# Performance work log

Measured on AMD Instinct MI355X. Metric: run time of the kernel, lower is better.

## Reference

```python
import jax, jax.numpy as jnp
import numpy as np

B, N, NB, C, CZ = 4, 1024, 32, 384, 128
EPS = 1e-6


def setup_inputs() -> dict:
    key = jax.random.key(0)
    k1, k2, k3, k4, k5 = jax.random.split(key, 5)
    s_i = jax.random.normal(k1, (B, N, C), dtype=jnp.float32)
    s_ij = jax.random.normal(k2, (B, N, NB, C), dtype=jnp.float32)
    m_ij = jnp.ones((B, N, NB), dtype=jnp.float32)
    z_ij = jax.random.normal(k3, (B, N, NB, CZ), dtype=jnp.float32)
    W_s = jax.random.normal(k4, (C, C), dtype=jnp.float32) / np.sqrt(C)
    W_z = jax.random.normal(k5, (CZ, C), dtype=jnp.float32) / np.sqrt(CZ)
    gamma = jnp.ones((C,), dtype=jnp.float32)
    beta = jnp.zeros((C,), dtype=jnp.float32)
    return {"s_i": s_i, "s_ij": s_ij, "m_ij": m_ij, "z_ij": z_ij,
            "W_s": W_s, "W_z": W_z, "gamma": gamma, "beta": beta}


def reference(s_i, s_ij, m_ij, z_ij, W_s, W_z, gamma, beta):
    # Dense projection of neighbor single act: (B,N,n,C) @ (C,C)
    s_proj = jnp.einsum('bnkc,cd->bnkd', s_ij, W_s)
    # subtract center single act
    diff = s_proj - s_i[..., None, :]
    # gate by projected pair act: (B,N,n,Cz) @ (Cz,C)
    gate = jnp.einsum('bnkz,zd->bnkd', z_ij, W_z)
    msg = diff * gate
    # masked sum over neighbor axis
    s_new = jnp.sum(msg * m_ij[..., None], axis=-2)  # (B,N,C)
    # layernorm over last axis
    mu = jnp.mean(s_new, axis=-1, keepdims=True)
    var = jnp.mean(jnp.square(s_new - mu), axis=-1, keepdims=True)
    s_new = (s_new - mu) * jax.lax.rsqrt(var + EPS) * gamma + beta
    return s_new
```

## Files before the change

kernel.cpp:

```cpp
#include <hip/hip_runtime.h>
#include <hip/hip_bf16.h>

#define B_ 4
#define N_ 1024
#define NB_ 32
#define C_ 384
#define CZ_ 128
#define NSITES (B_ * N_)
#define EPSV 1e-6f
#define PAD 40
#define SPB 2
#define MR 64
#define THREADS 512

typedef unsigned short u16;
typedef unsigned int u32;
typedef __bf16 bf16x8 __attribute__((ext_vector_type(8)));
typedef float f32x4 __attribute__((ext_vector_type(4)));

__device__ __forceinline__ u16 f2bf(float f) {
    return __builtin_bit_cast(u16, __float2bfloat16(f));
}
__device__ __forceinline__ u32 pk2(float lo, float hi) {
    return ((u32)f2bf(hi) << 16) | f2bf(lo);
}
__device__ __forceinline__ float bfbits2f(u16 u) {
    union { float f; u32 i; } x;
    x.i = ((u32)u) << 16;
    return x.f;
}

__global__ void prep_weights(const float* __restrict__ Ws, const float* __restrict__ Wz,
                             u16* __restrict__ Wts, u16* __restrict__ Wtz) {
    int idx = blockIdx.x * 256 + threadIdx.x;
    if (idx < C_ * C_) {
        int d = idx / C_, c = idx % C_;
        Wts[idx] = f2bf(Ws[c * C_ + d]);
    } else {
        int j = idx - C_ * C_;
        if (j < C_ * CZ_) {
            int d = j / CZ_, z = j % CZ_;
            Wtz[j] = f2bf(Wz[z * C_ + d]);
        }
    }
}

__global__ __launch_bounds__(THREADS, 4)
void fused_msg_kernel(const float* __restrict__ s_i,
                      const float* __restrict__ s_ij,
                      const float* __restrict__ m_ij,
                      const float* __restrict__ z_ij,
                      const u16* __restrict__ Wts,
                      const u16* __restrict__ Wtz,
                      const float* __restrict__ gamma,
                      const float* __restrict__ beta,
                      float* __restrict__ out) {
    __shared__ u16 ldsW[2][C_ * PAD];
    __shared__ u16 ldsA[2][MR * PAD];
    __shared__ float lds_snew[SPB * C_];

    const int tid = threadIdx.x;
    const int wave = tid >> 6;
    const int lane = tid & 63;
    const int q = lane >> 4;
    const int ln = lane & 15;
    const int mg = wave >> 2;
    const int cb = (wave & 3) * 96;

    const int site0 = blockIdx.x * SPB;
    const long rowbase = (long)site0 * NB_;

    const int arow = tid >> 3, aseg = tid & 7;
    const int wrow = tid >> 2, wseg = tid & 3;
    const int la_w = arow * PAD + aseg * 4;
    const int lw_w = wrow * PAD + wseg * 8;

    const float mv = m_ij[rowbase + lane];

    const f32x4 ZERO = {0.f, 0.f, 0.f, 0.f};
    f32x4 acc[2][6];
    #pragma unroll
    for (int mt = 0; mt < 2; ++mt)
        #pragma unroll
        for (int nt = 0; nt < 6; ++nt)
            acc[mt][nt] = ZERO;

    float4 ra;
    uint4 rw0, rw1, rw2;

    {
        const int kd = CZ_;
        const float* ap = z_ij + (rowbase + arow) * kd + aseg * 4;
        const u16* wp = Wtz + wrow * kd + wseg * 8;
        const int ws1 = 128 * kd, ws2 = 256 * kd;

        ra = *reinterpret_cast<const float4*>(ap);
        rw0 = *reinterpret_cast<const uint4*>(wp);
        rw1 = *reinterpret_cast<const uint4*>(wp + ws1);
        rw2 = *reinterpret_cast<const uint4*>(wp + ws2);
        ap += 32; wp += 32;
        {
            uint2 a2 = {pk2(ra.x, ra.y), pk2(ra.z, ra.w)};
            *reinterpret_cast<uint2*>(&ldsA[0][la_w]) = a2;
            *reinterpret_cast<uint4*>(&ldsW[0][lw_w]) = rw0;
            *reinterpret_cast<uint4*>(&ldsW[0][lw_w + 128 * PAD]) = rw1;
            *reinterpret_cast<uint4*>(&ldsW[0][lw_w + 256 * PAD]) = rw2;
        }
        __syncthreads();

        #pragma unroll 2
        for (int c = 0; c < 4; ++c) {
            if (c + 1 < 4) {
                ra = *reinterpret_cast<const float4*>(ap);
                rw0 = *reinterpret_cast<const uint4*>(wp);
                rw1 = *reinterpret_cast<const uint4*>(wp + ws1);
                rw2 = *reinterpret_cast<const uint4*>(wp + ws2);
                ap += 32; wp += 32;
            }
            const u16* lA = ldsA[c & 1];
            const u16* lW = ldsW[c & 1];
            bf16x8 a0 = *reinterpret_cast<const bf16x8*>(&lA[(mg * 32 + ln) * PAD + q * 8]);
            bf16x8 a1 = *reinterpret_cast<const bf16x8*>(&lA[(mg * 32 + 16 + ln) * PAD + q * 8]);
            #pragma unroll
            for (int nt = 0; nt < 6; ++nt) {
                bf16x8 b = *reinterpret_cast<const bf16x8*>(&lW[(cb + nt * 16 + ln) * PAD + q * 8]);
                acc[0][nt] = __builtin_amdgcn_mfma_f32_16x16x32_bf16(a0, b, acc[0][nt], 0, 0, 0);
                acc[1][nt] = __builtin_amdgcn_mfma_f32_16x16x32_bf16(a1, b, acc[1][nt], 0, 0, 0);
            }
            if (c + 1 < 4) {
                int nb = (c + 1) & 1;
                uint2 a2 = {pk2(ra.x, ra.y), pk2(ra.z, ra.w)};
                *reinterpret_cast<uint2*>(&ldsA[nb][la_w]) = a2;
                *reinterpret_cast<uint4*>(&ldsW[nb][lw_w]) = rw0;
                *reinterpret_cast<uint4*>(&ldsW[nb][lw_w + 128 * PAD]) = rw1;
                *reinterpret_cast<uint4*>(&ldsW[nb][lw_w + 256 * PAD]) = rw2;
            }
            __syncthreads();
        }
    }

    u32 gateb[2][6][2];
    #pragma unroll
    for (int mt = 0; mt < 2; ++mt) {
        int rb = mg * 32 + mt * 16 + q * 4;
        float m0 = __shfl(mv, rb + 0, 64);
        float m1 = __shfl(mv, rb + 1, 64);
        float m2 = __shfl(mv, rb + 2, 64);
        float m3 = __shfl(mv, rb + 3, 64);
        #pragma unroll
        for (int nt = 0; nt < 6; ++nt) {
            gateb[mt][nt][0] = pk2(acc[mt][nt][0] * m0, acc[mt][nt][1] * m1);
            gateb[mt][nt][1] = pk2(acc[mt][nt][2] * m2, acc[mt][nt][3] * m3);
            acc[mt][nt] = ZERO;
        }
    }

    {
        const int kd = C_;
        const float* ap = s_ij + (rowbase + arow) * kd + aseg * 4;
        const u16* wp = Wts + wrow * kd + wseg * 8;
        const int ws1 = 128 * kd, ws2 = 256 * kd;

        ra = *reinterpret_cast<const float4*>(ap);
        rw0 = *reinterpret_cast<const uint4*>(wp);
        rw1 = *reinterpret_cast<const uint4*>(wp + ws1);
        rw2 = *reinterpret_cast<const uint4*>(wp + ws2);
        ap += 32; wp += 32;
        {
            uint2 a2 = {pk2(ra.x, ra.y), pk2(ra.z, ra.w)};
            *reinterpret_cast<uint2*>(&ldsA[0][la_w]) = a2;
            *reinterpret_cast<uint4*>(&ldsW[0][lw_w]) = rw0;
            *reinterpret_cast<uint4*>(&ldsW[0][lw_w + 128 * PAD]) = rw1;
            *reinterpret_cast<uint4*>(&ldsW[0][lw_w + 256 * PAD]) = rw2;
        }
        __syncthreads();

        #pragma unroll 2
        for (int c = 0; c < 12; ++c) {
            if (c + 1 < 12) {
                ra = *reinterpret_cast<const float4*>(ap);
                rw0 = *reinterpret_cast<const uint4*>(wp);
                rw1 = *reinterpret_cast<const uint4*>(wp + ws1);
                rw2 = *reinterpret_cast<const uint4*>(wp + ws2);
                ap += 32; wp += 32;
            }
            const u16* lA = ldsA[c & 1];
            const u16* lW = ldsW[c & 1];
            bf16x8 a0 = *reinterpret_cast<const bf16x8*>(&lA[(mg * 32 + ln) * PAD + q * 8]);
            bf16x8 a1 = *reinterpret_cast<const bf16x8*>(&lA[(mg * 32 + 16 + ln) * PAD + q * 8]);
            #pragma unroll
            for (int nt = 0; nt < 6; ++nt) {
                bf16x8 b = *reinterpret_cast<const bf16x8*>(&lW[(cb + nt * 16 + ln) * PAD + q * 8]);
                acc[0][nt] = __builtin_amdgcn_mfma_f32_16x16x32_bf16(a0, b, acc[0][nt], 0, 0, 0);
                acc[1][nt] = __builtin_amdgcn_mfma_f32_16x16x32_bf16(a1, b, acc[1][nt], 0, 0, 0);
            }
            if (c + 1 < 12) {
                int nb = (c + 1) & 1;
                uint2 a2 = {pk2(ra.x, ra.y), pk2(ra.z, ra.w)};
                *reinterpret_cast<uint2*>(&ldsA[nb][la_w]) = a2;
                *reinterpret_cast<uint4*>(&ldsW[nb][lw_w]) = rw0;
                *reinterpret_cast<uint4*>(&ldsW[nb][lw_w + 128 * PAD]) = rw1;
                *reinterpret_cast<uint4*>(&ldsW[nb][lw_w + 256 * PAD]) = rw2;
            }
            __syncthreads();
        }
    }

    #pragma unroll
    for (int nt = 0; nt < 6; ++nt) {
        int col = cb + nt * 16 + ln;
        float si = s_i[(long)(site0 + mg) * C_ + col];
        float p = 0.f;
        #pragma unroll
        for (int mt = 0; mt < 2; ++mt) {
            #pragma unroll
            for (int r = 0; r < 4; ++r) {
                float g = bfbits2f((u16)(gateb[mt][nt][r >> 1] >> ((r & 1) * 16)));
                p += (acc[mt][nt][r] - si) * g;
            }
        }
        p += __shfl_xor(p, 16, 64);
        p += __shfl_xor(p, 32, 64);
        if (q == 0) lds_snew[mg * C_ + col] = p;
    }
    __syncthreads();

    if (wave < SPB) {
        const int site = wave;
        float v[6];
        float sum = 0.f, sumsq = 0.f;
        #pragma unroll
        for (int i = 0; i < 6; ++i) {
            v[i] = lds_snew[site * C_ + lane + i * 64];
            sum += v[i];
            sumsq += v[i] * v[i];
        }
        #pragma unroll
        for (int off = 32; off >= 1; off >>= 1) {
            sum += __shfl_xor(sum, off, 64);
            sumsq += __shfl_xor(sumsq, off, 64);
        }
        float mu = sum * (1.f / C_);
        float var = sumsq * (1.f / C_) - mu * mu;
        float rs = rsqrtf(var + EPSV);
        #pragma unroll
        for (int i = 0; i < 6; ++i) {
            int col = lane + i * 64;
            out[(long)(site0 + site) * C_ + col] = (v[i] - mu) * rs * gamma[col] + beta[col];
        }
    }
}

extern "C" void kernel_launch(void* const* d_in, const int* in_sizes, int n_in,
                              void* d_out, int out_size, void* d_ws, size_t ws_size,
                              hipStream_t stream) {
    (void)in_sizes; (void)n_in; (void)out_size; (void)ws_size;
    const float* s_i   = (const float*)d_in[0];
    const float* s_ij  = (const float*)d_in[1];
    const float* m_ij  = (const float*)d_in[2];
    const float* z_ij  = (const float*)d_in[3];
    const float* W_s   = (const float*)d_in[4];
    const float* W_z   = (const float*)d_in[5];
    const float* gamma = (const float*)d_in[6];
    const float* beta  = (const float*)d_in[7];
    float* out = (float*)d_out;

    u16* wts = (u16*)d_ws;
    u16* wtz = wts + C_ * C_;

    int prep_elems = C_ * C_ + C_ * CZ_;
    prep_weights<<<(prep_elems + 255) / 256, 256, 0, stream>>>(W_s, W_z, wts, wtz);
    fused_msg_kernel<<<NSITES / SPB, THREADS, 0, stream>>>(s_i, s_ij, m_ij, z_ij, wts, wtz,
                                                           gamma, beta, out);
}
```

Measured before the change: 438.7 us.

## Stage weights via global_load_lds and load activations straight into MFMA registers

Weights are pre-laid-out in chunked, fragment-order bf16 so each K-chunk can be copied into LDS with direct global-to-LDS loads, with no register round trip. Activation fragments are read from global straight into registers in MFMA operand layout and converted there, removing the LDS staging of the A operand and its bank traffic. LDS use per block drops, which may help occupancy. In exchange each lane now issues scattered per-row float4 loads of the activations, which may coalesce worse than the earlier contiguous row loads.

Measured after the change: 468.1 us. 6.7% more time.

```diff
diff --git a/kernel.cpp b/kernel.cpp
--- a/kernel.cpp
+++ b/kernel.cpp
@@ -8,10 +8,11 @@
 #define CZ_ 128
 #define NSITES (B_ * N_)
 #define EPSV 1e-6f
-#define PAD 40
 #define SPB 2
-#define MR 64
 #define THREADS 512
+#define WCHUNK_B 24576
+#define NKS 12
+#define NKZ 4
 
 typedef unsigned short u16;
 typedef unsigned int u32;
@@ -29,18 +30,31 @@
     x.i = ((u32)u) << 16;
     return x.f;
 }
+__device__ __forceinline__ bf16x8 mk8(float4 lo, float4 hi) {
+    union { u32 u[4]; bf16x8 v; } x;
+    x.u[0] = pk2(lo.x, lo.y); x.u[1] = pk2(lo.z, lo.w);
+    x.u[2] = pk2(hi.x, hi.y); x.u[3] = pk2(hi.z, hi.w);
+    return x.v;
+}
 
 __global__ void prep_weights(const float* __restrict__ Ws, const float* __restrict__ Wz,
-                             u16* __restrict__ Wts, u16* __restrict__ Wtz) {
+                             u16* __restrict__ wsS, u16* __restrict__ wsZ) {
     int idx = blockIdx.x * 256 + threadIdx.x;
-    if (idx < C_ * C_) {
-        int d = idx / C_, c = idx % C_;
-        Wts[idx] = f2bf(Ws[c * C_ + d]);
+    const int NS = NKS * 4 * C_ * 8;
+    if (idx < NS) {
+        int e = idx & 7, t = idx >> 3;
+        int d = t % C_, u = t / C_;
+        int q = u & 3, c = u >> 2;
+        int k = c * 32 + q * 8 + e;
+        wsS[idx] = f2bf(Ws[k * C_ + d]);
     } else {
-        int j = idx - C_ * C_;
-        if (j < C_ * CZ_) {
-            int d = j / CZ_, z = j % CZ_;
-            Wtz[j] = f2bf(Wz[z * C_ + d]);
+        int j = idx - NS;
+        if (j < NKZ * 4 * C_ * 8) {
+            int e = j & 7, t = j >> 3;
+            int d = t % C_, u = t / C_;
+            int q = u & 3, c = u >> 2;
+            int k = c * 32 + q * 8 + e;
+            wsZ[j] = f2bf(Wz[k * C_ + d]);
         }
     }
 }
@@ -50,13 +64,12 @@
                       const float* __restrict__ s_ij,
                       const float* __restrict__ m_ij,
                       const float* __restrict__ z_ij,
-                      const u16* __restrict__ Wts,
-                      const u16* __restrict__ Wtz,
+                      const u16* __restrict__ wsS,
+                      const u16* __restrict__ wsZ,
                       const float* __restrict__ gamma,
                       const float* __restrict__ beta,
                       float* __restrict__ out) {
-    __shared__ u16 ldsW[2][C_ * PAD];
-    __shared__ u16 ldsA[2][MR * PAD];
+    __shared__ u16 ldsW[2][WCHUNK_B / 2];
     __shared__ float lds_snew[SPB * C_];
 
     const int tid = threadIdx.x;
@@ -69,11 +82,7 @@
 
     const int site0 = blockIdx.x * SPB;
     const long rowbase = (long)site0 * NB_;
-
-    const int arow = tid >> 3, aseg = tid & 7;
-    const int wrow = tid >> 2, wseg = tid & 3;
-    const int la_w = arow * PAD + aseg * 4;
-    const int lw_w = wrow * PAD + wseg * 8;
+    const long arow0 = rowbase + mg * 32 + ln;
 
     const float mv = m_ij[rowbase + lane];
 
@@ -85,59 +94,61 @@
         for (int nt = 0; nt < 6; ++nt)
             acc[mt][nt] = ZERO;
 
-    float4 ra;
-    uint4 rw0, rw1, rw2;
-
-    {
-        const int kd = CZ_;
-        const float* ap = z_ij + (rowbase + arow) * kd + aseg * 4;
-        const u16* wp = Wtz + wrow * kd + wseg * 8;
-        const int ws1 = 128 * kd, ws2 = 256 * kd;
-
-        ra = *reinterpret_cast<const float4*>(ap);
-        rw0 = *reinterpret_cast<const uint4*>(wp);
-        rw1 = *reinterpret_cast<const uint4*>(wp + ws1);
-        rw2 = *reinterpret_cast<const uint4*>(wp + ws2);
-        ap += 32; wp += 32;
-        {
-            uint2 a2 = {pk2(ra.x, ra.y), pk2(ra.z, ra.w)};
-            *reinterpret_cast<uint2*>(&ldsA[0][la_w]) = a2;
-            *reinterpret_cast<uint4*>(&ldsW[0][lw_w]) = rw0;
-            *reinterpret_cast<uint4*>(&ldsW[0][lw_w + 128 * PAD]) = rw1;
-            *reinterpret_cast<uint4*>(&ldsW[0][lw_w + 256 * PAD]) = rw2;
-        }
+    float4 ra[2][4];
+    const int ldsq = q * (C_ * 8);
+
+#define STAGE_W(wsbase, c, buf) do {                                          \
+        const char* _s = (const char*)(wsbase) + (c) * WCHUNK_B;              \
+        char* _d = (char*)&ldsW[(buf)][0];                                    \
+        _Pragma("unroll")                                                     \
+        for (int _i = 0; _i < 3; ++_i) {                                      \
+            int _o = _i * 8192 + tid * 16;                                    \
+            __builtin_amdgcn_global_load_lds(                                 \
+                (const __attribute__((address_space(1))) void*)(_s + _o),     \
+                (__attribute__((address_space(3))) void*)(_d + _o),           \
+                16, 0, 0);                                                    \
+        }                                                                     \
+    } while (0)
+
+#define LOAD_A(base, kd, c, sl) do {                                          \
+        const float* _p0 = (base) + arow0 * (kd) + (c) * 32 + q * 8;          \
+        const float* _p1 = _p0 + 16 * (kd);                                   \
+        ra[sl][0] = *reinterpret_cast<const float4*>(_p0);                    \
+        ra[sl][1] = *reinterpret_cast<const float4*>(_p0 + 4);                \
+        ra[sl][2] = *reinterpret_cast<const float4*>(_p1);                    \
+        ra[sl][3] = *reinterpret_cast<const float4*>(_p1 + 4);                \
+    } while (0)
+
+#define COMPUTE(sl) do {                                                      \
+        bf16x8 _a0 = mk8(ra[sl][0], ra[sl][1]);                               \
+        bf16x8 _a1 = mk8(ra[sl][2], ra[sl][3]);                               \
+        const u16* _lw = &ldsW[sl][ldsq];                                     \
+        _Pragma("unroll")                                                     \
+        for (int _nt = 0; _nt < 6; ++_nt) {                                   \
+            bf16x8 _b = *reinterpret_cast<const bf16x8*>(                     \
+                _lw + (cb + _nt * 16 + ln) * 8);                              \
+            acc[0][_nt] = __builtin_amdgcn_mfma_f32_16x16x32_bf16(            \
+                _a0, _b, acc[0][_nt], 0, 0, 0);                               \
+            acc[1][_nt] = __builtin_amdgcn_mfma_f32_16x16x32_bf16(            \
+                _a1, _b, acc[1][_nt], 0, 0, 0);                               \
+        }                                                                     \
+    } while (0)
+
+    STAGE_W(wsZ, 0, 0);
+    LOAD_A(z_ij, CZ_, 0, 0);
+    __syncthreads();
+    #pragma unroll
+    for (int c = 0; c < NKZ; ++c) {
+        if (c + 1 < NKZ) {
+            STAGE_W(wsZ, c + 1, (c + 1) & 1);
+            LOAD_A(z_ij, CZ_, c + 1, (c + 1) & 1);
+        }
+        COMPUTE(c & 1);
         __syncthreads();
-
-        #pragma unroll 2
-        for (int c = 0; c < 4; ++c) {
-            if (c + 1 < 4) {
-                ra = *reinterpret_cast<const float4*>(ap);
-                rw0 = *reinterpret_cast<const uint4*>(wp);
-                rw1 = *reinterpret_cast<const uint4*>(wp + ws1);
-                rw2 = *reinterpret_cast<const uint4*>(wp + ws2);
-                ap += 32; wp += 32;
-            }
-            const u16* lA = ldsA[c & 1];
-            const u16* lW = ldsW[c & 1];
-            bf16x8 a0 = *reinterpret_cast<const bf16x8*>(&lA[(mg * 32 + ln) * PAD + q * 8]);
-            bf16x8 a1 = *reinterpret_cast<const bf16x8*>(&lA[(mg * 32 + 16 + ln) * PAD + q * 8]);
-            #pragma unroll
-            for (int nt = 0; nt < 6; ++nt) {
-                bf16x8 b = *reinterpret_cast<const bf16x8*>(&lW[(cb + nt * 16 + ln) * PAD + q * 8]);
-                acc[0][nt] = __builtin_amdgcn_mfma_f32_16x16x32_bf16(a0, b, acc[0][nt], 0, 0, 0);
-                acc[1][nt] = __builtin_amdgcn_mfma_f32_16x16x32_bf16(a1, b, acc[1][nt], 0, 0, 0);
-            }
-            if (c + 1 < 4) {
-                int nb = (c + 1) & 1;
-                uint2 a2 = {pk2(ra.x, ra.y), pk2(ra.z, ra.w)};
-                *reinterpret_cast<uint2*>(&ldsA[nb][la_w]) = a2;
-                *reinterpret_cast<uint4*>(&ldsW[nb][lw_w]) = rw0;
-                *reinterpret_cast<uint4*>(&ldsW[nb][lw_w + 128 * PAD]) = rw1;
-                *reinterpret_cast<uint4*>(&ldsW[nb][lw_w + 256 * PAD]) = rw2;
-            }
-            __syncthreads();
-        }
-    }
+    }
+
+    STAGE_W(wsS, 0, 0);
+    LOAD_A(s_ij, C_, 0, 0);
 
     u32 gateb[2][6][2];
     #pragma unroll
@@ -154,57 +165,21 @@
             acc[mt][nt] = ZERO;
         }
     }
-
-    {
-        const int kd = C_;
-        const float* ap = s_ij + (rowbase + arow) * kd + aseg * 4;
-        const u16* wp = Wts + wrow * kd + wseg * 8;
-        const int ws1 = 128 * kd, ws2 = 256 * kd;
-
-        ra = *reinterpret_cast<const float4*>(ap);
-        rw0 = *reinterpret_cast<const uint4*>(wp);
-        rw1 = *reinterpret_cast<const uint4*>(wp + ws1);
-        rw2 = *reinterpret_cast<const uint4*>(wp + ws2);
-        ap += 32; wp += 32;
-        {
-            uint2 a2 = {pk2(ra.x, ra.y), pk2(ra.z, ra.w)};
-            *reinterpret_cast<uint2*>(&ldsA[0][la_w]) = a2;
-            *reinterpret_cast<uint4*>(&ldsW[0][lw_w]) = rw0;
-            *reinterpret_cast<uint4*>(&ldsW[0][lw_w + 128 * PAD]) = rw1;
-            *reinterpret_cast<uint4*>(&ldsW[0][lw_w + 256 * PAD]) = rw2;
-        }
+    __syncthreads();
+
+    #pragma unroll
+    for (int c = 0; c < NKS; ++c) {
+        if (c + 1 < NKS) {
+            STAGE_W(wsS, c + 1, (c + 1) & 1);
+            LOAD_A(s_ij, C_, c + 1, (c + 1) & 1);
+        }
+        COMPUTE(c & 1);
         __syncthreads();
-
-        #pragma unroll 2
-        for (int c = 0; c < 12; ++c) {
-            if (c + 1 < 12) {
-                ra = *reinterpret_cast<const float4*>(ap);
-                rw0 = *reinterpret_cast<const uint4*>(wp);
-                rw1 = *reinterpret_cast<const uint4*>(wp + ws1);
-                rw2 = *reinterpret_cast<const uint4*>(wp + ws2);
-                ap += 32; wp += 32;
-            }
-            const u16* lA = ldsA[c & 1];
-            const u16* lW = ldsW[c & 1];
-            bf16x8 a0 = *reinterpret_cast<const bf16x8*>(&lA[(mg * 32 + ln) * PAD + q * 8]);
-            bf16x8 a1 = *reinterpret_cast<const bf16x8*>(&lA[(mg * 32 + 16 + ln) * PAD + q * 8]);
-            #pragma unroll
-            for (int nt = 0; nt < 6; ++nt) {
-                bf16x8 b = *reinterpret_cast<const bf16x8*>(&lW[(cb + nt * 16 + ln) * PAD + q * 8]);
-                acc[0][nt] = __builtin_amdgcn_mfma_f32_16x16x32_bf16(a0, b, acc[0][nt], 0, 0, 0);
-                acc[1][nt] = __builtin_amdgcn_mfma_f32_16x16x32_bf16(a1, b, acc[1][nt], 0, 0, 0);
-            }
-            if (c + 1 < 12) {
-                int nb = (c + 1) & 1;
-                uint2 a2 = {pk2(ra.x, ra.y), pk2(ra.z, ra.w)};
-                *reinterpret_cast<uint2*>(&ldsA[nb][la_w]) = a2;
-                *reinterpret_cast<uint4*>(&ldsW[nb][lw_w]) = rw0;
-                *reinterpret_cast<uint4*>(&ldsW[nb][lw_w + 128 * PAD]) = rw1;
-                *reinterpret_cast<uint4*>(&ldsW[nb][lw_w + 256 * PAD]) = rw2;
-            }
-            __syncthreads();
-        }
-    }
+    }
+
+#undef STAGE_W
+#undef LOAD_A
+#undef COMPUTE
 
     #pragma unroll
     for (int nt = 0; nt < 6; ++nt) {
@@ -265,11 +240,11 @@
     const float* beta  = (const float*)d_in[7];
     float* out = (float*)d_out;
 
-    u16* wts = (u16*)d_ws;
-    u16* wtz = wts + C_ * C_;
-
-    int prep_elems = C_ * C_ + C_ * CZ_;
-    prep_weights<<<(prep_elems + 255) / 256, 256, 0, stream>>>(W_s, W_z, wts, wtz);
-    fused_msg_kernel<<<NSITES / SPB, THREADS, 0, stream>>>(s_i, s_ij, m_ij, z_ij, wts, wtz,
-                                                           gamma, beta, out);
-}
+    u16* wsS = (u16*)d_ws;
+    u16* wsZ = wsS + NKS * 4 * C_ * 8;
+
+    int prep_elems = NKS * 4 * C_ * 8 + NKZ * 4 * C_ * 8;
+    prep_weights<<<(prep_elems + 255) / 256, 256, 0, stream>>>(W_s, W_z, wsS, wsZ);
+    fused_msg_kernel<<<NSITES / SPB, THREADS, 0, stream>>>(s_i, s_ij, m_ij, z_ij,
+                                                           wsS, wsZ, gamma, beta, out);
+}
```

## Pre-swizzle weights into MFMA fragment order and hoist s_ij prefetch over gate packing

Applied to the files above, without the earlier changes.

Weights are reordered at prep time into a chunk/quad/column/8-element layout, so each thread copies contiguous 16-byte runs from global to LDS and the MFMA B operands are read at unpadded contiguous offsets. The A tile in LDS is split into quad-planes with a small pad instead of the row PAD=40 layout. The first s_ij and W_s chunk loads are issued before the gate pack/mask step, so that latency overlaps the conversion work. This cuts LDS footprint and strided global weight reads, but it can change LDS bank-conflict behaviour.

Result: faster. 385.2 us (-12.2%).

```diff
diff --git a/kernel.cpp b/kernel.cpp
--- a/kernel.cpp
+++ b/kernel.cpp
@@ -8,10 +8,13 @@
 #define CZ_ 128
 #define NSITES (B_ * N_)
 #define EPSV 1e-6f
-#define PAD 40
 #define SPB 2
-#define MR 64
 #define THREADS 512
+#define NKZ 4
+#define NKS 12
+#define WCH_U16 12288
+#define APLANE 528
+#define ABUF_U16 (3 * APLANE + 512)
 
 typedef unsigned short u16;
 typedef unsigned int u32;
@@ -31,16 +34,23 @@
 }
 
 __global__ void prep_weights(const float* __restrict__ Ws, const float* __restrict__ Wz,
-                             u16* __restrict__ Wts, u16* __restrict__ Wtz) {
+                             u16* __restrict__ wsS, u16* __restrict__ wsZ) {
     int idx = blockIdx.x * 256 + threadIdx.x;
-    if (idx < C_ * C_) {
-        int d = idx / C_, c = idx % C_;
-        Wts[idx] = f2bf(Ws[c * C_ + d]);
+    const int NS = NKS * 4 * C_ * 8;
+    if (idx < NS) {
+        int e = idx & 7, t = idx >> 3;
+        int d = t % C_, u = t / C_;
+        int q = u & 3, c = u >> 2;
+        int k = c * 32 + q * 8 + e;
+        wsS[idx] = f2bf(Ws[k * C_ + d]);
     } else {
-        int j = idx - C_ * C_;
-        if (j < C_ * CZ_) {
-            int d = j / CZ_, z = j % CZ_;
-            Wtz[j] = f2bf(Wz[z * C_ + d]);
+        int j = idx - NS;
+        if (j < NKZ * 4 * C_ * 8) {
+            int e = j & 7, t = j >> 3;
+            int d = t % C_, u = t / C_;
+            int q = u & 3, c = u >> 2;
+            int k = c * 32 + q * 8 + e;
+            wsZ[j] = f2bf(Wz[k * C_ + d]);
         }
     }
 }
@@ -50,13 +60,13 @@
                       const float* __restrict__ s_ij,
                       const float* __restrict__ m_ij,
                       const float* __restrict__ z_ij,
-                      const u16* __restrict__ Wts,
-                      const u16* __restrict__ Wtz,
+                      const u16* __restrict__ wsS,
+                      const u16* __restrict__ wsZ,
                       const float* __restrict__ gamma,
                       const float* __restrict__ beta,
                       float* __restrict__ out) {
-    __shared__ u16 ldsW[2][C_ * PAD];
-    __shared__ u16 ldsA[2][MR * PAD];
+    __shared__ u16 ldsW[2][WCH_U16];
+    __shared__ u16 ldsA[2][ABUF_U16];
     __shared__ float lds_snew[SPB * C_];
 
     const int tid = threadIdx.x;
@@ -71,9 +81,8 @@
     const long rowbase = (long)site0 * NB_;
 
     const int arow = tid >> 3, aseg = tid & 7;
-    const int wrow = tid >> 2, wseg = tid & 3;
-    const int la_w = arow * PAD + aseg * 4;
-    const int lw_w = wrow * PAD + wseg * 8;
+    const int la_w = (aseg >> 1) * APLANE + arow * 8 + (aseg & 1) * 4;
+    const int lw_w = tid * 8;
 
     const float mv = m_ij[rowbase + lane];
 
@@ -88,56 +97,65 @@
     float4 ra;
     uint4 rw0, rw1, rw2;
 
+    const int ra0 = q * APLANE + (mg * 32 + ln) * 8;
+    const int wq0 = q * 3072;
+
     {
-        const int kd = CZ_;
-        const float* ap = z_ij + (rowbase + arow) * kd + aseg * 4;
-        const u16* wp = Wtz + wrow * kd + wseg * 8;
-        const int ws1 = 128 * kd, ws2 = 256 * kd;
+        const float* ap = z_ij + (rowbase + arow) * CZ_ + aseg * 4;
+        const u16* wp = wsZ + lw_w;
 
         ra = *reinterpret_cast<const float4*>(ap);
         rw0 = *reinterpret_cast<const uint4*>(wp);
-        rw1 = *reinterpret_cast<const uint4*>(wp + ws1);
-        rw2 = *reinterpret_cast<const uint4*>(wp + ws2);
-        ap += 32; wp += 32;
+        rw1 = *reinterpret_cast<const uint4*>(wp + 4096);
+        rw2 = *reinterpret_cast<const uint4*>(wp + 8192);
+        ap += 32; wp += WCH_U16;
         {
             uint2 a2 = {pk2(ra.x, ra.y), pk2(ra.z, ra.w)};
             *reinterpret_cast<uint2*>(&ldsA[0][la_w]) = a2;
             *reinterpret_cast<uint4*>(&ldsW[0][lw_w]) = rw0;
-            *reinterpret_cast<uint4*>(&ldsW[0][lw_w + 128 * PAD]) = rw1;
-            *reinterpret_cast<uint4*>(&ldsW[0][lw_w + 256 * PAD]) = rw2;
+            *reinterpret_cast<uint4*>(&ldsW[0][lw_w + 4096]) = rw1;
+            *reinterpret_cast<uint4*>(&ldsW[0][lw_w + 8192]) = rw2;
         }
         __syncthreads();
 
         #pragma unroll 2
-        for (int c = 0; c < 4; ++c) {
-            if (c + 1 < 4) {
+        for (int c = 0; c < NKZ; ++c) {
+            if (c + 1 < NKZ) {
                 ra = *reinterpret_cast<const float4*>(ap);
                 rw0 = *reinterpret_cast<const uint4*>(wp);
-                rw1 = *reinterpret_cast<const uint4*>(wp + ws1);
-                rw2 = *reinterpret_cast<const uint4*>(wp + ws2);
-                ap += 32; wp += 32;
+                rw1 = *reinterpret_cast<const uint4*>(wp + 4096);
+                rw2 = *reinterpret_cast<const uint4*>(wp + 8192);
+                ap += 32; wp += WCH_U16;
             }
             const u16* lA = ldsA[c & 1];
             const u16* lW = ldsW[c & 1];
-            bf16x8 a0 = *reinterpret_cast<const bf16x8*>(&lA[(mg * 32 + ln) * PAD + q * 8]);
-            bf16x8 a1 = *reinterpret_cast<const bf16x8*>(&lA[(mg * 32 + 16 + ln) * PAD + q * 8]);
+            bf16x8 a0 = *reinterpret_cast<const bf16x8*>(&lA[ra0]);
+            bf16x8 a1 = *reinterpret_cast<const bf16x8*>(&lA[ra0 + 128]);
             #pragma unroll
             for (int nt = 0; nt < 6; ++nt) {
-                bf16x8 b = *reinterpret_cast<const bf16x8*>(&lW[(cb + nt * 16 + ln) * PAD + q * 8]);
+                bf16x8 b = *reinterpret_cast<const bf16x8*>(&lW[wq0 + (cb + nt * 16 + ln) * 8]);
                 acc[0][nt] = __builtin_amdgcn_mfma_f32_16x16x32_bf16(a0, b, acc[0][nt], 0, 0, 0);
                 acc[1][nt] = __builtin_amdgcn_mfma_f32_16x16x32_bf16(a1, b, acc[1][nt], 0, 0, 0);
             }
-            if (c + 1 < 4) {
+            if (c + 1 < NKZ) {
                 int nb = (c + 1) & 1;
                 uint2 a2 = {pk2(ra.x, ra.y), pk2(ra.z, ra.w)};
                 *reinterpret_cast<uint2*>(&ldsA[nb][la_w]) = a2;
                 *reinterpret_cast<uint4*>(&ldsW[nb][lw_w]) = rw0;
-                *reinterpret_cast<uint4*>(&ldsW[nb][lw_w + 128 * PAD]) = rw1;
-                *reinterpret_cast<uint4*>(&ldsW[nb][lw_w + 256 * PAD]) = rw2;
+                *reinterpret_cast<uint4*>(&ldsW[nb][lw_w + 4096]) = rw1;
+                *reinterpret_cast<uint4*>(&ldsW[nb][lw_w + 8192]) = rw2;
             }
             __syncthreads();
         }
     }
+
+    const float* ap = s_ij + (rowbase + arow) * C_ + aseg * 4;
+    const u16* wp = wsS + lw_w;
+    ra = *reinterpret_cast<const float4*>(ap);
+    rw0 = *reinterpret_cast<const uint4*>(wp);
+    rw1 = *reinterpret_cast<const uint4*>(wp + 4096);
+    rw2 = *reinterpret_cast<const uint4*>(wp + 8192);
+    ap += 32; wp += WCH_U16;
 
     u32 gateb[2][6][2];
     #pragma unroll
@@ -156,51 +174,41 @@
     }
 
     {
-        const int kd = C_;
-        const float* ap = s_ij + (rowbase + arow) * kd + aseg * 4;
-        const u16* wp = Wts + wrow * kd + wseg * 8;
-        const int ws1 = 128 * kd, ws2 = 256 * kd;
-
-        ra = *reinterpret_cast<const float4*>(ap);
-        rw0 = *reinterpret_cast<const uint4*>(wp);
-        rw1 = *reinterpret_cast<const uint4*>(wp + ws1);
-        rw2 = *reinterpret_cast<const uint4*>(wp + ws2);
-        ap += 32; wp += 32;
-        {
-            uint2 a2 = {pk2(ra.x, ra.y), pk2(ra.z, ra.w)};
-            *reinterpret_cast<uint2*>(&ldsA[0][la_w]) = a2;
-            *reinterpret_cast<uint4*>(&ldsW[0][lw_w]) = rw0;
-            *reinterpret_cast<uint4*>(&ldsW[0][lw_w + 128 * PAD]) = rw1;
-            *reinterpret_cast<uint4*>(&ldsW[0][lw_w + 256 * PAD]) = rw2;
-        }
-        __syncthreads();
-
+        uint2 a2 = {pk2(ra.x, ra.y), pk2(ra.z, ra.w)};
+        *reinterpret_cast<uint2*>(&ldsA[0][la_w]) = a2;
+        *reinterpret_cast<uint4*>(&ldsW[0][lw_w]) = rw0;
+        *reinterpret_cast<uint4*>(&ldsW[0][lw_w + 4096]) = rw1;
+        *reinterpret_cast<uint4*>(&ldsW[0][lw_w + 8192]) = rw2;
+    }
+    __syncthreads();
+
+    {
         #pragma unroll 2
-        for (int c = 0; c < 12; ++c) {
-            if (c + 1 < 12) {
+        for (int c = 0; c < NKS; ++c) {
+            if (c + 1 < NKS) {
                 ra = *reinterpret_cast<const float4*>(ap);
                 rw0 = *reinterpret_cast<const uint4*>(wp);
-                rw1 = *reinterpret_cast<const uint4*>(wp + ws1);
-                rw2 = *reinterpret_cast<const uint4*>(wp + ws2);
-                ap += 32; wp += 32;
+                rw1 = *reinterpret_cast<const uint4*>(wp + 4096);
+                rw2 = *reinterpret_cast<const uint4*>(wp + 8192);
+                ap += 32; wp += WCH_U16;
             }
             const u16* lA = ldsA[c & 1];
             const u16* lW = ldsW[c & 1];
-            bf16x8 a0 = *reinterpret_cast<const bf16x8*>(&lA[(mg * 32 + ln) * PAD + q * 8]);
-            bf16x8 a1 = *reinterpret_cast<const bf16x8*>(&lA[(mg * 32 + 16 + ln) * PAD + q * 8]);
+            bf16x8 a0 = *reinterpret_cast<const bf16x8*>(&lA[ra0]);
+            bf16x8 a1 = *reinterpret_cast<const bf16x8*>(&lA[ra0 + 128]);
             #pragma unroll
             for (int nt = 0; nt < 6; ++nt) {
-                bf16x8 b = *reinterpret_cast<const bf16x8*>(&lW[(cb + nt * 16 + ln) * PAD + q * 8]);
+                bf16x8 b = *reinterpret_cast<const bf16x8*>(&lW[wq0 + (cb + nt * 16 + ln) * 8]);
                 acc[0][nt] = __builtin_amdgcn_mfma_f32_16x16x32_bf16(a0, b, acc[0][nt], 0, 0, 0);
                 acc[1][nt] = __builtin_amdgcn_mfma_f32_16x16x32_bf16(a1, b, acc[1][nt], 0, 0, 0);
             }
-            if (c + 1 < 12) {
+            if (c + 1 < NKS) {
                 int nb = (c + 1) & 1;
                 uint2 a2 = {pk2(ra.x, ra.y), pk2(ra.z, ra.w)};
                 *reinterpret_cast<uint2*>(&ldsA[nb][la_w]) = a2;
                 *reinterpret_cast<uint4*>(&ldsW[nb][lw_w]) = rw0;
-                *reinterpret_cast<uint4*>(&ldsW[nb][lw_w + 128 * PAD]) = rw1;
-                *reinterpret_cast<uint4*>(&ldsW[nb][lw_w + 256 * PAD]) = rw2;
+                *reinterpret_cast<uint4*>(&ldsW[nb][lw_w + 4096]) = rw1;
+                *reinterpret_cast<uint4*>(&ldsW[nb][lw_w + 8192]) = rw2;
             }
             __syncthreads();
         }
@@ -265,11 +273,11 @@
     const float* beta  = (const float*)d_in[7];
     float* out = (float*)d_out;
 
-    u16* wts = (u16*)d_ws;
-    u16* wtz = wts + C_ * C_;
-
-    int prep_elems = C_ * C_ + C_ * CZ_;
-    prep_weights<<<(prep_elems + 255) / 256, 256, 0, stream>>>(W_s, W_z, wts, wtz);
-    fused_msg_kernel<<<NSITES / SPB, THREADS, 0, stream>>>(s_i, s_ij, m_ij, z_ij, wts, wtz,
-                                                           gamma, beta, out);
-}
+    u16* wsS = (u16*)d_ws;
+    u16* wsZ = wsS + NKS * 4 * C_ * 8;
+
+    int prep_elems = NKS * 4 * C_ * 8 + NKZ * 4 * C_ * 8;
+    prep_weights<<<(prep_elems + 255) / 256, 256, 0, stream>>>(W_s, W_z, wsS, wsZ);
+    fused_msg_kernel<<<NSITES / SPB, THREADS, 0, stream>>>(s_i, s_ij, m_ij, z_ij,
+                                                           wsS, wsZ, gamma, beta, out);
+}
```
